# Kernel tuning notes

Hardware: AMD Instinct MI355X
Metric: run time of the kernel (lower is better)

## Reference

```python
import jax, jax.numpy as jnp
import numpy as np

EMBED_DIM = 1024
NUM_HEADS = 16
HEAD_DIM = EMBED_DIM // NUM_HEADS
MLP_HIDDEN = 4096


def layer_norm(x, gamma, beta, eps=1e-5):
    mu = jnp.mean(x, axis=-1, keepdims=True)
    var = jnp.var(x, axis=-1, keepdims=True)
    return (x - mu) / jnp.sqrt(var + eps) * gamma + beta


def setup_inputs() -> dict:
    key = jax.random.key(0)
    ks = jax.random.split(key, 16)
    d, h = EMBED_DIM, MLP_HIDDEN
    s = 0.02
    inp = {
        "x": jax.random.normal(ks[0], (2, 2048, d), dtype=jnp.float32),
        "ln1_g": jnp.ones((d,), jnp.float32),
        "ln1_b": jnp.zeros((d,), jnp.float32),
        "ln2_g": jnp.ones((d,), jnp.float32),
        "ln2_b": jnp.zeros((d,), jnp.float32),
        "Wq": jax.random.normal(ks[1], (d, d), jnp.float32) * s,
        "bq": jnp.zeros((d,), jnp.float32),
        "Wk": jax.random.normal(ks[2], (d, d), jnp.float32) * s,
        "bk": jnp.zeros((d,), jnp.float32),
        "Wv": jax.random.normal(ks[3], (d, d), jnp.float32) * s,
        "bv": jnp.zeros((d,), jnp.float32),
        "Wo": jax.random.normal(ks[4], (d, d), jnp.float32) * s,
        "bo": jnp.zeros((d,), jnp.float32),
        "W1": jax.random.normal(ks[5], (d, h), jnp.float32) * s,
        "b1": jnp.zeros((h,), jnp.float32),
        "W2": jax.random.normal(ks[6], (h, d), jnp.float32) * s,
        "b2": jnp.zeros((d,), jnp.float32),
    }
    return inp


def reference(x, ln1_g, ln1_b, ln2_g, ln2_b, Wq, bq, Wk, bk, Wv, bv, Wo, bo, W1, b1, W2, b2):
    B, T, C = x.shape
    H, Dh = NUM_HEADS, HEAD_DIM
    # attention branch
    xn = layer_norm(x, ln1_g, ln1_b)
    q = (xn @ Wq + bq).reshape(B, T, H, Dh).transpose(0, 2, 1, 3)  # [B,H,T,Dh]
    k = (xn @ Wk + bk).reshape(B, T, H, Dh).transpose(0, 2, 1, 3)
    v = (xn @ Wv + bv).reshape(B, T, H, Dh).transpose(0, 2, 1, 3)
    scores = jnp.einsum('bhtd,bhsd->bhts', q, k) / jnp.sqrt(jnp.float32(Dh))
    attn = jax.nn.softmax(scores, axis=-1)
    out = jnp.einsum('bhts,bhsd->bhtd', attn, v)
    out = out.transpose(0, 2, 1, 3).reshape(B, T, C)
    x = x + out @ Wo + bo
    # MLP branch
    xn2 = layer_norm(x, ln2_g, ln2_b)
    x = x + jax.nn.relu(xn2 @ W1 + b1) @ W2 + b2
    return x
```

## Files before the change

kernel.cpp:

```cpp
#include <hip/hip_runtime.h>

typedef float f32x4 __attribute__((ext_vector_type(4)));
typedef __bf16 bf16x8 __attribute__((ext_vector_type(8)));

constexpr int TT   = 2048;
constexpr int CC   = 1024;
constexpr int HIDN = 4096;
constexpr int MM   = 4096;
constexpr int NQKV = 3072;

union U84 { uint32_t u[4]; bf16x8 v; };

__device__ inline uint32_t cvt_pk_bf16(float lo, float hi) {
  uint32_t r;
  asm("v_cvt_pk_bf16_f32 %0, %1, %2" : "=v"(r) : "v"(lo), "v"(hi));
  return r;
}
__device__ inline ushort f2bf(float f) { return (ushort)(cvt_pk_bf16(f, 0.f) & 0xffffu); }
__device__ inline float bfbits2f(uint32_t bits) {
  union { uint32_t u; float f; } c; c.u = bits; return c.f;
}
__device__ inline float exp2_fast(float x) {
  float r;
  asm("v_exp_f32 %0, %1" : "=v"(r) : "v"(x));
  return r;
}

#define AS1C(p) ((__attribute__((address_space(1))) void*)(p))
#define AS3(p)  ((__attribute__((address_space(3))) void*)(p))

__global__ __launch_bounds__(256) void prep_weights(const float* __restrict__ Wq,
                                                    const float* __restrict__ Wk,
                                                    const float* __restrict__ Wv,
                                                    const float* __restrict__ Wo,
                                                    const float* __restrict__ W1,
                                                    const float* __restrict__ W2,
                                                    const float* __restrict__ bq,
                                                    const float* __restrict__ bk,
                                                    const float* __restrict__ bv,
                                                    const float* __restrict__ x,
                                                    const float* __restrict__ g1,
                                                    const float* __restrict__ b1v,
                                                    ushort* __restrict__ WqkvT,
                                                    ushort* __restrict__ WoT,
                                                    ushort* __restrict__ W1T,
                                                    ushort* __restrict__ W2T,
                                                    float* __restrict__ Bqkv,
                                                    ushort* __restrict__ Xn) {
  const int id = blockIdx.x;
  const int t = threadIdx.x;
  if (id >= 12300) {
    const int row = id - 12300;
    float4 v = reinterpret_cast<const float4*>(x + (size_t)row * CC)[t];
    float s  = v.x + v.y + v.z + v.w;
    float ss = v.x * v.x + v.y * v.y + v.z * v.z + v.w * v.w;
#pragma unroll
    for (int off = 32; off; off >>= 1) {
      s  += __shfl_down(s, off);
      ss += __shfl_down(ss, off);
    }
    __shared__ float red[16];
    const int wid = t >> 6, lane = t & 63;
    if (lane == 0) { red[wid] = s; red[8 + wid] = ss; }
    __syncthreads();
    if (t == 0) {
      red[0] = red[0] + red[1] + red[2] + red[3];
      red[8] = red[8] + red[9] + red[10] + red[11];
    }
    __syncthreads();
    const float mu   = red[0] * (1.0f / CC);
    const float var  = red[8] * (1.0f / CC) - mu * mu;
    const float rstd = rsqrtf(var + 1e-5f);
    float4 gg = reinterpret_cast<const float4*>(g1)[t];
    float4 bb = reinterpret_cast<const float4*>(b1v)[t];
    uint2 st;
    st.x = cvt_pk_bf16((v.x - mu) * rstd * gg.x + bb.x, (v.y - mu) * rstd * gg.y + bb.y);
    st.y = cvt_pk_bf16((v.z - mu) * rstd * gg.z + bb.z, (v.w - mu) * rstd * gg.w + bb.w);
    *reinterpret_cast<uint2*>(Xn + (size_t)row * CC + t * 4) = st;
    return;
  }
  if (id >= 12288) {
    const int i = (id - 12288) * 256 + t;
    Bqkv[i] = (i < 1024) ? bq[i] : ((i < 2048) ? bk[i - 1024] : bv[i - 2048]);
    return;
  }
  const float* W; ushort* out; int Kd, Nd, bx, by, rowOff = 0;
  if (id < 4096) {
    const int which = id >> 10, sub = id & 1023;
    bx = sub & 31; by = sub >> 5; Kd = 1024; Nd = 1024;
    if (which == 0)      { W = Wq; out = WqkvT; rowOff = 0; }
    else if (which == 1) { W = Wk; out = WqkvT; rowOff = 1024; }
    else if (which == 2) { W = Wv; out = WqkvT; rowOff = 2048; }
    else                 { W = Wo; out = WoT; }
  } else if (id < 8192) {
    const int sub = id - 4096; bx = sub & 127; by = sub >> 7;
    W = W1; out = W1T; Kd = 1024; Nd = 4096;
  } else {
    const int sub = id - 8192; bx = sub & 31; by = sub >> 5;
    W = W2; out = W2T; Kd = 4096; Nd = 1024;
  }
  const int n0 = bx * 32, k0 = by * 32;
  __shared__ float Ts[32][33];
  {
    const int r = t >> 3, cb = (t & 7) * 4;
    float4 v = *reinterpret_cast<const float4*>(W + (size_t)(k0 + r) * Nd + n0 + cb);
    Ts[r][cb + 0] = v.x; Ts[r][cb + 1] = v.y; Ts[r][cb + 2] = v.z; Ts[r][cb + 3] = v.w;
  }
  __syncthreads();
  {
    const int nl = t >> 3, kb = (t & 7) * 4;
    uint2 st;
    st.x = cvt_pk_bf16(Ts[kb + 0][nl], Ts[kb + 1][nl]);
    st.y = cvt_pk_bf16(Ts[kb + 2][nl], Ts[kb + 3][nl]);
    *reinterpret_cast<uint2*>(out + (size_t)(rowOff + n0 + nl) * Kd + k0 + kb) = st;
  }
}

template <bool RELU, bool VOUT, bool PARTIAL>
__global__ __launch_bounds__(512, 2) void gemm_8w(const ushort* __restrict__ A,
                                                  const ushort* __restrict__ Bt,
                                                  const float* __restrict__ bias,
                                                  ushort* __restrict__ outp,
                                                  ushort* __restrict__ Vt,
                                                  ushort* __restrict__ P1,
                                                  ushort* __restrict__ P2,
                                                  ushort* __restrict__ P3,
                                                  int N, int K, int Kchunk) {
  __shared__ ushort lds[49152];
  const int t = threadIdx.x, lane = t & 63, w = t >> 6;
  const int g = lane >> 4, i16 = lane & 15;
  const int wr = w >> 2, wc = w & 3;
  const int nwg  = gridDim.x * gridDim.y;
  const int orig = blockIdx.y * gridDim.x + blockIdx.x;
  const int sw   = (orig & 7) * (nwg >> 3) + (orig >> 3);
  const int row0 = (sw / gridDim.x) * 256, col0 = (sw % gridDim.x) * 256;
  const int kstart = PARTIAL ? blockIdx.z * Kchunk : 0;
  const int NT = (PARTIAL ? Kchunk : K) >> 5;
  ushort* __restrict__ Out = outp;
  if (PARTIAL) Out = (blockIdx.z == 0) ? outp : (blockIdx.z == 1) ? P1
              : (blockIdx.z == 2) ? P2 : P3;

  const int c1 = t, c2 = t + 512;
  const int r1 = c1 >> 2, s1 = (c1 & 3) ^ ((r1 >> 1) & 3);
  const int r2 = c2 >> 2, s2 = (c2 & 3) ^ ((r2 >> 1) & 3);
  const ushort* aG1 = A + (size_t)(row0 + r1) * K + kstart + s1 * 8;
  const ushort* aG2 = A + (size_t)(row0 + r2) * K + kstart + s2 * 8;
  const ushort* bG1 = Bt + (size_t)(col0 + r1) * K + kstart + s1 * 8;
  const ushort* bG2 = Bt + (size_t)(col0 + r2) * K + kstart + s2 * 8;

  int aoff[8], boff[4];
#pragma unroll
  for (int mf = 0; mf < 8; ++mf) {
    const int R = wr * 128 + mf * 16 + i16;
    aoff[mf] = R * 64 + ((g ^ ((R >> 1) & 3)) << 4);
  }
#pragma unroll
  for (int nf = 0; nf < 4; ++nf) {
    const int Cn = wc * 64 + nf * 16 + i16;
    boff[nf] = Cn * 64 + ((g ^ ((Cn >> 1) & 3)) << 4);
  }

  f32x4 acc[8][4] = {};

  auto STAGE = [&](int bi, int kt) {
    char* aB = (char*)lds + bi * 32768;
    char* bB = aB + 16384;
    const int ko = kt * 32;
    __builtin_amdgcn_global_load_lds(AS1C(aG1 + ko), AS3(aB + w * 1024), 16, 0, 0);
    __builtin_amdgcn_global_load_lds(AS1C(aG2 + ko), AS3(aB + 8192 + w * 1024), 16, 0, 0);
    __builtin_amdgcn_global_load_lds(AS1C(bG1 + ko), AS3(bB + w * 1024), 16, 0, 0);
    __builtin_amdgcn_global_load_lds(AS1C(bG2 + ko), AS3(bB + 8192 + w * 1024), 16, 0, 0);
  };

  STAGE(0, 0);
  if (NT > 1) STAGE(1, 1);

  for (int kt = 0; kt < NT; ++kt) {
    const int cur = kt % 3;
    if (kt + 2 < NT) STAGE((kt + 2) % 3, kt + 2);
    if (kt + 2 < NT)      asm volatile("s_waitcnt vmcnt(8)" ::: "memory");
    else if (kt + 1 < NT) asm volatile("s_waitcnt vmcnt(4)" ::: "memory");
    else                  asm volatile("s_waitcnt vmcnt(0)" ::: "memory");
    asm volatile("s_barrier" ::: "memory");
    __builtin_amdgcn_sched_barrier(0);

    const char* aB = (const char*)lds + cur * 32768;
    const char* bB = aB + 16384;
    bf16x8 b4[4], a4[4];
#pragma unroll
    for (int nf = 0; nf < 4; ++nf) b4[nf] = *reinterpret_cast<const bf16x8*>(bB + boff[nf]);
#pragma unroll
    for (int mf = 0; mf < 4; ++mf) a4[mf] = *reinterpret_cast<const bf16x8*>(aB + aoff[mf]);
    __builtin_amdgcn_s_setprio(1);
#pragma unroll
    for (int mf = 0; mf < 4; ++mf)
#pragma unroll
      for (int nf = 0; nf < 4; ++nf)
        acc[mf][nf] = __builtin_amdgcn_mfma_f32_16x16x32_bf16(a4[mf], b4[nf], acc[mf][nf], 0, 0, 0);
    __builtin_amdgcn_s_setprio(0);
    asm volatile("s_barrier" ::: "memory");
    __builtin_amdgcn_sched_barrier(0);
#pragma unroll
    for (int mf = 0; mf < 4; ++mf) a4[mf] = *reinterpret_cast<const bf16x8*>(aB + aoff[mf + 4]);
    __builtin_amdgcn_s_setprio(1);
#pragma unroll
    for (int mf = 0; mf < 4; ++mf)
#pragma unroll
      for (int nf = 0; nf < 4; ++nf)
        acc[mf + 4][nf] = __builtin_amdgcn_mfma_f32_16x16x32_bf16(a4[mf], b4[nf], acc[mf + 4][nf], 0, 0, 0);
    __builtin_amdgcn_s_setprio(0);
    asm volatile("s_barrier" ::: "memory");
    __builtin_amdgcn_sched_barrier(0);
  }

  const int qcol0 = col0 + wc * 64;

  if (VOUT && qcol0 >= 2048) {
#pragma unroll
    for (int nf = 0; nf < 4; ++nf) {
      const int ncol = qcol0 + nf * 16 + i16;
      const float bb = bias[ncol];
      const int d = ncol - 2048;
      const int hh = d >> 6, dd = d & 63;
#pragma unroll
      for (int mf = 0; mf < 8; ++mf) {
        const int mrow = row0 + wr * 128 + mf * 16 + 4 * g;
        const int bb_ = mrow >> 11, tok = mrow & 2047;
        uint2 st;
        st.x = cvt_pk_bf16(acc[mf][nf][0] + bb, acc[mf][nf][1] + bb);
        st.y = cvt_pk_bf16(acc[mf][nf][2] + bb, acc[mf][nf][3] + bb);
        *reinterpret_cast<uint2*>(Vt + (size_t)((bb_ * 16 + hh) * 64 + dd) * TT + tok) = st;
      }
    }
    return;
  }

  float* Lf = (float*)((char*)lds + w * 4096);
  const int rr2 = lane >> 2, q = lane & 3;
#pragma unroll
  for (int mf = 0; mf < 8; ++mf) {
#pragma unroll
    for (int nf = 0; nf < 4; ++nf)
#pragma unroll
      for (int r = 0; r < 4; ++r) {
        const int row = 4 * g + r;
        Lf[row * 64 + ((16 * nf + i16) ^ ((row & 7) << 2))] = acc[mf][nf][r];
      }
    asm volatile("s_waitcnt lgkmcnt(0)" ::: "memory");
    uint32_t u[8];
#pragma unroll
    for (int j = 0; j < 4; ++j) {
      f32x4 v = *reinterpret_cast<const f32x4*>(Lf + rr2 * 64 + ((q * 16 + 4 * j) ^ ((rr2 & 7) << 2)));
      float e0 = v[0], e1 = v[1], e2 = v[2], e3 = v[3];
      if (!PARTIAL) {
        const float4 b4 = *reinterpret_cast<const float4*>(bias + qcol0 + q * 16 + 4 * j);
        e0 += b4.x; e1 += b4.y; e2 += b4.z; e3 += b4.w;
        if (RELU) {
          e0 = fmaxf(e0, 0.f); e1 = fmaxf(e1, 0.f);
          e2 = fmaxf(e2, 0.f); e3 = fmaxf(e3, 0.f);
        }
      }
      u[2 * j + 0] = cvt_pk_bf16(e0, e1);
      u[2 * j + 1] = cvt_pk_bf16(e2, e3);
    }
    const int mrow = row0 + wr * 128 + mf * 16 + rr2;
    ushort* orow = Out + (size_t)mrow * N + qcol0 + q * 16;
    uint4 s0; s0.x = u[0]; s0.y = u[1]; s0.z = u[2]; s0.w = u[3];
    uint4 s1; s1.x = u[4]; s1.y = u[5]; s1.z = u[6]; s1.w = u[7];
    *reinterpret_cast<uint4*>(orow) = s0;
    *reinterpret_cast<uint4*>(orow + 8) = s1;
    asm volatile("s_waitcnt lgkmcnt(0)" ::: "memory");
  }
}

__global__ __launch_bounds__(256) void gemm_splitk(const ushort* __restrict__ A,
                                                   const ushort* __restrict__ Bt,
                                                   ushort* __restrict__ P0,
                                                   ushort* __restrict__ P1,
                                                   ushort* __restrict__ P2,
                                                   ushort* __restrict__ P3,
                                                   int N, int K, int Kchunk) {
  __shared__ ushort Smem[8192];
  ushort* Asm = Smem;
  ushort* Bsm = Smem + 4096;
  const int t = threadIdx.x;
  const int lane = t & 63, w = t >> 6;
  const int g = lane >> 4, i16 = lane & 15;
  const int wrow = w >> 1, wcol = w & 1;
  const int nwg  = gridDim.x * gridDim.y;
  const int orig = blockIdx.y * gridDim.x + blockIdx.x;
  const int sw   = (orig & 7) * (nwg >> 3) + (orig >> 3);
  const int row0 = (sw / gridDim.x) * 128, col0 = (sw % gridDim.x) * 128;
  const int kstart = blockIdx.z * Kchunk;
  ushort* __restrict__ P = (blockIdx.z == 0) ? P0 : (blockIdx.z == 1) ? P1
                          : (blockIdx.z == 2) ? P2 : P3;

  f32x4 acc[4][4] = {};

  const int srow = t >> 2, sc = (t & 3) * 8;
  const ushort* aS1 = A + (size_t)(row0 + srow) * K + sc;
  const ushort* aS2 = A + (size_t)(row0 + 64 + srow) * K + sc;
  const ushort* bS1 = Bt + (size_t)(col0 + srow) * K + sc;
  const ushort* bS2 = Bt + (size_t)(col0 + 64 + srow) * K + sc;
  char* aL1 = (char*)Asm + w * 1024;
  char* aL2 = (char*)Asm + 4096 + w * 1024;
  char* bL1 = (char*)Bsm + w * 1024;
  char* bL2 = (char*)Bsm + 4096 + w * 1024;

  for (int k0 = kstart; k0 < kstart + Kchunk; k0 += 32) {
    __syncthreads();
    __builtin_amdgcn_global_load_lds(AS1C(aS1 + k0), AS3(aL1), 16, 0, 0);
    __builtin_amdgcn_global_load_lds(AS1C(aS2 + k0), AS3(aL2), 16, 0, 0);
    __builtin_amdgcn_global_load_lds(AS1C(bS1 + k0), AS3(bL1), 16, 0, 0);
    __builtin_amdgcn_global_load_lds(AS1C(bS2 + k0), AS3(bL2), 16, 0, 0);
    __syncthreads();

    bf16x8 a4[4], b4[4];
#pragma unroll
    for (int mf = 0; mf < 4; ++mf) {
      const int r = wrow * 64 + mf * 16 + i16;
      a4[mf] = *reinterpret_cast<const bf16x8*>((const char*)Asm + r * 64 + g * 16);
    }
#pragma unroll
    for (int nf = 0; nf < 4; ++nf) {
      const int c = wcol * 64 + nf * 16 + i16;
      b4[nf] = *reinterpret_cast<const bf16x8*>((const char*)Bsm + c * 64 + g * 16);
    }
#pragma unroll
    for (int mf = 0; mf < 4; ++mf)
#pragma unroll
      for (int nf = 0; nf < 4; ++nf)
        acc[mf][nf] = __builtin_amdgcn_mfma_f32_16x16x32_bf16(a4[mf], b4[nf], acc[mf][nf], 0, 0, 0);
  }

  __syncthreads();

  float* Lf = (float*)((char*)Smem + w * 4096);
  const int qcol0 = col0 + wcol * 64;
  const int rr = lane >> 2, q = lane & 3;
#pragma unroll
  for (int mf = 0; mf < 4; ++mf) {
#pragma unroll
    for (int nf = 0; nf < 4; ++nf)
#pragma unroll
      for (int r = 0; r < 4; ++r) {
        const int row = 4 * g + r;
        Lf[row * 64 + ((16 * nf + i16) ^ ((row & 7) << 2))] = acc[mf][nf][r];
      }
    asm volatile("s_waitcnt lgkmcnt(0)" ::: "memory");
    uint32_t u[8];
#pragma unroll
    for (int j = 0; j < 4; ++j) {
      f32x4 v = *reinterpret_cast<const f32x4*>(Lf + rr * 64 + ((q * 16 + 4 * j) ^ ((rr & 7) << 2)));
      u[2 * j + 0] = cvt_pk_bf16(v[0], v[1]);
      u[2 * j + 1] = cvt_pk_bf16(v[2], v[3]);
    }
    const int mrow = row0 + wrow * 64 + mf * 16 + rr;
    ushort* orow = P + (size_t)mrow * N + qcol0 + q * 16;
    uint4 s0; s0.x = u[0]; s0.y = u[1]; s0.z = u[2]; s0.w = u[3];
    uint4 s1; s1.x = u[4]; s1.y = u[5]; s1.z = u[6]; s1.w = u[7];
    *reinterpret_cast<uint4*>(orow) = s0;
    *reinterpret_cast<uint4*>(orow + 8) = s1;
    asm volatile("s_waitcnt lgkmcnt(0)" ::: "memory");
  }
}

__device__ inline float bfsum4(uint32_t a, uint32_t b, uint32_t c, uint32_t d, bool hi) {
  if (hi) return bfbits2f(a & 0xffff0000u) + bfbits2f(b & 0xffff0000u) +
                 bfbits2f(c & 0xffff0000u) + bfbits2f(d & 0xffff0000u);
  return bfbits2f(a << 16) + bfbits2f(b << 16) + bfbits2f(c << 16) + bfbits2f(d << 16);
}

__global__ __launch_bounds__(256) void reduce_wo_ln(const ushort* __restrict__ P0,
                                                    const ushort* __restrict__ P1,
                                                    const ushort* __restrict__ P2,
                                                    const ushort* __restrict__ P3,
                                                    const float* __restrict__ x,
                                                    const float* __restrict__ bo,
                                                    const float* __restrict__ g,
                                                    const float* __restrict__ b,
                                                    float* __restrict__ X1f,
                                                    ushort* __restrict__ Xn) {
  const int row = blockIdx.x, t = threadIdx.x;
  const size_t off = (size_t)row * CC + t * 4;
  float4 v  = *reinterpret_cast<const float4*>(x + off);
  const uint2 q0 = *reinterpret_cast<const uint2*>(P0 + off);
  const uint2 q1 = *reinterpret_cast<const uint2*>(P1 + off);
  const uint2 q2 = *reinterpret_cast<const uint2*>(P2 + off);
  const uint2 q3 = *reinterpret_cast<const uint2*>(P3 + off);
  float4 bb = reinterpret_cast<const float4*>(bo)[t];
  v.x += bfsum4(q0.x, q1.x, q2.x, q3.x, false) + bb.x;
  v.y += bfsum4(q0.x, q1.x, q2.x, q3.x, true)  + bb.y;
  v.z += bfsum4(q0.y, q1.y, q2.y, q3.y, false) + bb.z;
  v.w += bfsum4(q0.y, q1.y, q2.y, q3.y, true)  + bb.w;
  *reinterpret_cast<float4*>(X1f + off) = v;

  float s  = v.x + v.y + v.z + v.w;
  float ss = v.x * v.x + v.y * v.y + v.z * v.z + v.w * v.w;
#pragma unroll
  for (int o = 32; o; o >>= 1) {
    s  += __shfl_down(s, o);
    ss += __shfl_down(ss, o);
  }
  __shared__ float red[16];
  const int wid = t >> 6, lane = t & 63;
  if (lane == 0) { red[wid] = s; red[8 + wid] = ss; }
  __syncthreads();
  if (t == 0) {
    red[0] = red[0] + red[1] + red[2] + red[3];
    red[8] = red[8] + red[9] + red[10] + red[11];
  }
  __syncthreads();
  const float mu   = red[0] * (1.0f / CC);
  const float var  = red[8] * (1.0f / CC) - mu * mu;
  const float rstd = rsqrtf(var + 1e-5f);
  float4 gg = reinterpret_cast<const float4*>(g)[t];
  float4 lb = reinterpret_cast<const float4*>(b)[t];
  uint2 st;
  st.x = cvt_pk_bf16((v.x - mu) * rstd * gg.x + lb.x, (v.y - mu) * rstd * gg.y + lb.y);
  st.y = cvt_pk_bf16((v.z - mu) * rstd * gg.z + lb.z, (v.w - mu) * rstd * gg.w + lb.w);
  *reinterpret_cast<uint2*>(Xn + off) = st;
}

__global__ __launch_bounds__(256) void reduce_fc2(const ushort* __restrict__ P0,
                                                  const ushort* __restrict__ P1,
                                                  const ushort* __restrict__ P2,
                                                  const ushort* __restrict__ P3,
                                                  const float* __restrict__ X1,
                                                  const float* __restrict__ b2,
                                                  float* __restrict__ out) {
  const int row = blockIdx.x, t = threadIdx.x;
  const size_t off = (size_t)row * CC + t * 4;
  float4 v  = *reinterpret_cast<const float4*>(X1 + off);
  const uint2 q0 = *reinterpret_cast<const uint2*>(P0 + off);
  const uint2 q1 = *reinterpret_cast<const uint2*>(P1 + off);
  const uint2 q2 = *reinterpret_cast<const uint2*>(P2 + off);
  const uint2 q3 = *reinterpret_cast<const uint2*>(P3 + off);
  float4 bb = reinterpret_cast<const float4*>(b2)[t];
  v.x += bfsum4(q0.x, q1.x, q2.x, q3.x, false) + bb.x;
  v.y += bfsum4(q0.x, q1.x, q2.x, q3.x, true)  + bb.y;
  v.z += bfsum4(q0.y, q1.y, q2.y, q3.y, false) + bb.z;
  v.w += bfsum4(q0.y, q1.y, q2.y, q3.y, true)  + bb.w;
  *reinterpret_cast<float4*>(out + off) = v;
}

__global__ __launch_bounds__(512, 4) void attn_partial(const ushort* __restrict__ qkv,
                                                       const ushort* __restrict__ Vt,
                                                       ushort* __restrict__ O0,
                                                       ushort* __restrict__ O1,
                                                       float2* __restrict__ ml) {
  __shared__ ushort Ks[2][4096];
  __shared__ ushort Vs[2][4096];
  __shared__ uint32_t Ps[8][16][36];
  const int t = threadIdx.x, lane = t & 63, w = t >> 6;
  const int g = lane >> 4, iq = lane & 15;
  const int flat = blockIdx.x;
  const int work = (flat & 7) * 64 + (flat >> 3);
  const int bh = work >> 4;
  const int rem = work & 15;
  const int z = rem >> 3;
  const int qt = rem & 7;
  const int b = bh >> 4, h = bh & 15;
  ushort* __restrict__ Obuf = z ? O1 : O0;

  bf16x8 qfrag[2][2];
#pragma unroll
  for (int qh = 0; qh < 2; ++qh) {
    const ushort* qrow = qkv + (size_t)(b * TT + qt * 256 + w * 32 + qh * 16 + iq) * NQKV + h * 64;
    const float qs = 0.125f * 1.44269504f;
#pragma unroll
    for (int kk = 0; kk < 2; ++kk) {
      uint4 raw = *reinterpret_cast<const uint4*>(qrow + kk * 32 + g * 8);
      uint32_t rr[4] = {raw.x, raw.y, raw.z, raw.w};
      U84 tmp;
#pragma unroll
      for (int c = 0; c < 4; ++c) {
        float lo = bfbits2f(rr[c] << 16) * qs;
        float hi = bfbits2f(rr[c] & 0xffff0000u) * qs;
        tmp.u[c] = cvt_pk_bf16(lo, hi);
      }
      qfrag[qh][kk] = tmp.v;
    }
  }

  const int sr1 = t >> 3, sc1 = t & 7;
  const int csw = (sc1 ^ (sr1 & 7)) * 8;
  const ushort* kbase = qkv + 1024 + h * 64;
  const ushort* vbase = Vt + (size_t)(bh * 64) * TT;

  auto STAGE = [&](int bi, int kt) {
    const size_t tok = (size_t)(b * TT + kt * 64);
    __builtin_amdgcn_global_load_lds(AS1C(kbase + (tok + sr1) * NQKV + csw),
                                     AS3((char*)&Ks[bi][0] + w * 1024), 16, 0, 0);
    __builtin_amdgcn_global_load_lds(AS1C(vbase + (size_t)sr1 * TT + kt * 64 + csw),
                                     AS3((char*)&Vs[bi][0] + w * 1024), 16, 0, 0);
  };

  uint32_t (*pw)[36] = Ps[w];
  const int wsw = (iq & 8) << 1;
  const int xsb = wsw << 2;
  const char* prow = (const char*)&pw[iq][0];

  float mrun[2] = {-3e38f, -3e38f}, lrun[2] = {0.f, 0.f};
  f32x4 ot[2][4] = {};

  const int kt0 = z * 16, ktE = kt0 + 16;
  STAGE(0, kt0);

  for (int kt = kt0; kt < ktE; ++kt) {
    const int cur = kt & 1;
    if (kt + 1 < ktE) {
      STAGE(cur ^ 1, kt + 1);
      asm volatile("s_waitcnt vmcnt(2)" ::: "memory");
    } else {
      asm volatile("s_waitcnt vmcnt(0)" ::: "memory");
    }
    asm volatile("s_barrier" ::: "memory");
    __builtin_amdgcn_sched_barrier(0);
    const char* Kc = (const char*)&Ks[cur][0];
    const char* Vc = (const char*)&Vs[cur][0];

#pragma unroll
    for (int qh = 0; qh < 2; ++qh) {
      f32x4 sfr[4] = {};
      __builtin_amdgcn_s_setprio(1);
#pragma unroll
      for (int kk = 0; kk < 2; ++kk)
#pragma unroll
        for (int jf = 0; jf < 4; ++jf) {
          const int row = iq + 16 * jf;
          const int off = row * 128 + ((kk * 64 + g * 16) ^ ((row & 7) << 4));
          bf16x8 a = *reinterpret_cast<const bf16x8*>(Kc + off);
          sfr[jf] = __builtin_amdgcn_mfma_f32_16x16x32_bf16(a, qfrag[qh][kk], sfr[jf], 0, 0, 0);
        }
      __builtin_amdgcn_s_setprio(0);

      float tm0 = fmaxf(fmaxf(sfr[0][0], sfr[0][1]), fmaxf(sfr[0][2], sfr[0][3]));
      float tm1 = fmaxf(fmaxf(sfr[1][0], sfr[1][1]), fmaxf(sfr[1][2], sfr[1][3]));
      float tm2 = fmaxf(fmaxf(sfr[2][0], sfr[2][1]), fmaxf(sfr[2][2], sfr[2][3]));
      float tm3 = fmaxf(fmaxf(sfr[3][0], sfr[3][1]), fmaxf(sfr[3][2], sfr[3][3]));
      float tmax = fmaxf(fmaxf(tm0, tm1), fmaxf(tm2, tm3));
      tmax = fmaxf(tmax, __shfl_xor(tmax, 16, 64));
      tmax = fmaxf(tmax, __shfl_xor(tmax, 32, 64));

      if (!__all(tmax <= mrun[qh] + 8.f)) {
        const float mnew  = fmaxf(mrun[qh], tmax);
        const float alpha = exp2_fast(mrun[qh] - mnew);
        lrun[qh] *= alpha;
#pragma unroll
        for (int df = 0; df < 4; ++df)
#pragma unroll
          for (int r = 0; r < 4; ++r) ot[qh][df][r] *= alpha;
        mrun[qh] = mnew;
      }

#pragma unroll
      for (int f = 0; f < 4; ++f) {
        float p0 = exp2_fast(sfr[f][0] - mrun[qh]);
        float p1 = exp2_fast(sfr[f][1] - mrun[qh]);
        float p2 = exp2_fast(sfr[f][2] - mrun[qh]);
        float p3 = exp2_fast(sfr[f][3] - mrun[qh]);
        lrun[qh] += (p0 + p1) + (p2 + p3);
        pw[iq][(8 * f + 2 * g + 0) ^ wsw] = cvt_pk_bf16(p0, p1);
        pw[iq][(8 * f + 2 * g + 1) ^ wsw] = cvt_pk_bf16(p2, p3);
      }
      asm volatile("s_waitcnt lgkmcnt(0)" ::: "memory");

      __builtin_amdgcn_s_setprio(1);
#pragma unroll
      for (int kk = 0; kk < 2; ++kk) {
        bf16x8 pb = *reinterpret_cast<const bf16x8*>(prow + ((kk * 64 + g * 16) ^ xsb));
#pragma unroll
        for (int df = 0; df < 4; ++df) {
          const int row = iq + 16 * df;
          const int off = row * 128 + ((kk * 64 + g * 16) ^ ((row & 7) << 4));
          bf16x8 a = *reinterpret_cast<const bf16x8*>(Vc + off);
          ot[qh][df] = __builtin_amdgcn_mfma_f32_16x16x32_bf16(a, pb, ot[qh][df], 0, 0, 0);
        }
      }
      __builtin_amdgcn_s_setprio(0);
    }

    asm volatile("s_barrier" ::: "memory");
    __builtin_amdgcn_sched_barrier(0);
  }

#pragma unroll
  for (int qh = 0; qh < 2; ++qh) {
    float l = lrun[qh];
    l += __shfl_xor(l, 16, 64);
    l += __shfl_xor(l, 32, 64);
    const int grow = b * TT + qt * 256 + w * 32 + qh * 16 + iq;
    const float inv = 1.f / l;
    ushort* orow = Obuf + (size_t)grow * CC + h * 64;
#pragma unroll
    for (int df = 0; df < 4; ++df) {
      uint2 st;
      st.x = cvt_pk_bf16(ot[qh][df][0] * inv, ot[qh][df][1] * inv);
      st.y = cvt_pk_bf16(ot[qh][df][2] * inv, ot[qh][df][3] * inv);
      *reinterpret_cast<uint2*>(orow + df * 16 + g * 4) = st;
    }
    if (g == 0) ml[(size_t)z * (MM * 16) + (size_t)grow * 16 + h] = make_float2(mrun[qh], l);
  }
}

__global__ __launch_bounds__(256) void attn_combine(const ushort* __restrict__ O0,
                                                    const ushort* __restrict__ O1,
                                                    const float2* __restrict__ ml,
                                                    ushort* __restrict__ attnb) {
  const int row = blockIdx.x, t = threadIdx.x;
  const int h = t >> 4;
  const float2 a = ml[(size_t)row * 16 + h];
  const float2 c = ml[(size_t)MM * 16 + (size_t)row * 16 + h];
  const float m  = fmaxf(a.x, c.x);
  const float w0 = exp2_fast(a.x - m) * a.y;
  const float w1 = exp2_fast(c.x - m) * c.y;
  const float inv = 1.f / (w0 + w1);
  const float s0 = w0 * inv, s1 = w1 * inv;
  const size_t off = (size_t)row * CC + t * 4;
  const uint2 r0 = *reinterpret_cast<const uint2*>(O0 + off);
  const uint2 r1 = *reinterpret_cast<const uint2*>(O1 + off);
  const float o0 = bfbits2f(r0.x << 16)         * s0 + bfbits2f(r1.x << 16)         * s1;
  const float o1 = bfbits2f(r0.x & 0xffff0000u) * s0 + bfbits2f(r1.x & 0xffff0000u) * s1;
  const float o2 = bfbits2f(r0.y << 16)         * s0 + bfbits2f(r1.y << 16)         * s1;
  const float o3 = bfbits2f(r0.y & 0xffff0000u) * s0 + bfbits2f(r1.y & 0xffff0000u) * s1;
  uint2 st;
  st.x = cvt_pk_bf16(o0, o1);
  st.y = cvt_pk_bf16(o2, o3);
  *reinterpret_cast<uint2*>(attnb + off) = st;
}

extern "C" void kernel_launch(void* const* d_in, const int* in_sizes, int n_in,
                              void* d_out, int out_size, void* d_ws, size_t ws_size,
                              hipStream_t stream) {
  const float* x     = (const float*)d_in[0];
  const float* ln1_g = (const float*)d_in[1];
  const float* ln1_b = (const float*)d_in[2];
  const float* ln2_g = (const float*)d_in[3];
  const float* ln2_b = (const float*)d_in[4];
  const float* Wq = (const float*)d_in[5];
  const float* bq = (const float*)d_in[6];
  const float* Wk = (const float*)d_in[7];
  const float* bk = (const float*)d_in[8];
  const float* Wv = (const float*)d_in[9];
  const float* bv = (const float*)d_in[10];
  const float* Wo = (const float*)d_in[11];
  const float* bo = (const float*)d_in[12];
  const float* W1 = (const float*)d_in[13];
  const float* b1 = (const float*)d_in[14];
  const float* W2 = (const float*)d_in[15];
  const float* b2 = (const float*)d_in[16];
  float* out = (float*)d_out;
  char* ws = (char*)d_ws;

  ushort* WqkvT = (ushort*)(ws + 0);
  ushort* WoT   = (ushort*)(ws + 6291456);
  ushort* W1T   = (ushort*)(ws + 8388608);
  ushort* W2T   = (ushort*)(ws + 16777216);
  float*  Bqkv  = (float*) (ws + 25165824);
  ushort* Xn    = (ushort*)(ws + 25178112);
  ushort* Attn  = (ushort*)(ws + 33566720);
  float*  X1f   = (float*) (ws + 41955328);
  ushort* Qkv   = (ushort*)(ws + 58732544);
  ushort* Vtb   = (ushort*)(ws + 83898368);
  ushort* Hid   = (ushort*)(ws + 58732544);
  ushort* OP0   = (ushort*)(ws + 41955328);
  ushort* OP1   = (ushort*)(ws + 50343936);
  float2* mlbuf = (float2*)(ws + 0);
  ushort* WoP0  = (ushort*)(ws + 58732544);
  ushort* WoP1  = (ushort*)(ws + 67121152);
  ushort* WoP2  = (ushort*)(ws + 75509760);
  ushort* WoP3  = (ushort*)(ws + 83898368);
  ushort* F2P0  = (ushort*)(ws + 0);
  ushort* F2P1  = (ushort*)(ws + 8388608);
  ushort* F2P2  = (ushort*)(ws + 25178112);
  ushort* F2P3  = (ushort*)(ws + 33566720);

  const dim3 blk(256);

  prep_weights<<<dim3(16396), blk, 0, stream>>>(Wq, Wk, Wv, Wo, W1, W2, bq, bk, bv,
                                                x, ln1_g, ln1_b,
                                                WqkvT, WoT, W1T, W2T, Bqkv, Xn);
  gemm_8w<false, true, false><<<dim3(12, 16), dim3(512), 0, stream>>>(
      Xn, WqkvT, Bqkv, Qkv, Vtb, nullptr, nullptr, nullptr, NQKV, 1024, 0);
  attn_partial<<<dim3(512), dim3(512), 0, stream>>>(Qkv, Vtb, OP0, OP1, mlbuf);
  attn_combine<<<dim3(MM), blk, 0, stream>>>(OP0, OP1, mlbuf, Attn);
  gemm_splitk<<<dim3(8, 32, 4), blk, 0, stream>>>(Attn, WoT, WoP0, WoP1, WoP2, WoP3, 1024, 1024, 256);
  reduce_wo_ln<<<dim3(MM), blk, 0, stream>>>(WoP0, WoP1, WoP2, WoP3, x, bo, ln2_g, ln2_b, X1f, Xn);
  gemm_8w<true, false, false><<<dim3(16, 16), dim3(512), 0, stream>>>(
      Xn, W1T, b1, Hid, nullptr, nullptr, nullptr, nullptr, HIDN, 1024, 0);
  gemm_8w<false, false, true><<<dim3(4, 16, 4), dim3(512), 0, stream>>>(
      Hid, W2T, nullptr, F2P0, nullptr, F2P1, F2P2, F2P3, 1024, 4096, 1024);
  reduce_fc2<<<dim3(MM), blk, 0, stream>>>(F2P0, F2P1, F2P2, F2P3, X1f, b2, out);
}
```

Before: 255.9 us.

## Load attention K/V fragments directly from global memory, dropping LDS staging

Removes the double-buffered LDS staging of K and V tiles along with its barriers. Each wave now loads its K and V MFMA fragments straight from global memory into registers, and both query halves share one set of K fragments for the score MFMAs. This cuts LDS traffic and block-wide synchronisation, but each of the 8 waves issues its own redundant global loads of the same K/V tile. It also adds register pressure and loses the prefetch overlap that the double buffer provided.

Measured after the change: 343.3 us. 34.1% more time.

```diff
diff --git a/kernel.cpp b/kernel.cpp
--- a/kernel.cpp
+++ b/kernel.cpp
@@ -449,8 +449,6 @@
                                                        ushort* __restrict__ O0,
                                                        ushort* __restrict__ O1,
                                                        float2* __restrict__ ml) {
-  __shared__ ushort Ks[2][4096];
-  __shared__ ushort Vs[2][4096];
   __shared__ uint32_t Ps[8][16][36];
   const int t = threadIdx.x, lane = t & 63, w = t >> 6;
   const int g = lane >> 4, iq = lane & 15;
@@ -483,18 +481,8 @@
     }
   }
 
-  const int sr1 = t >> 3, sc1 = t & 7;
-  const int csw = (sc1 ^ (sr1 & 7)) * 8;
-  const ushort* kbase = qkv + 1024 + h * 64;
-  const ushort* vbase = Vt + (size_t)(bh * 64) * TT;
-
-  auto STAGE = [&](int bi, int kt) {
-    const size_t tok = (size_t)(b * TT + kt * 64);
-    __builtin_amdgcn_global_load_lds(AS1C(kbase + (tok + sr1) * NQKV + csw),
-                                     AS3((char*)&Ks[bi][0] + w * 1024), 16, 0, 0);
-    __builtin_amdgcn_global_load_lds(AS1C(vbase + (size_t)sr1 * TT + kt * 64 + csw),
-                                     AS3((char*)&Vs[bi][0] + w * 1024), 16, 0, 0);
-  };
+  const ushort* kW = qkv + 1024 + h * 64 + (size_t)(b * TT + iq) * NQKV + g * 8;
+  const ushort* vW = Vt + (size_t)(bh * 64 + iq) * TT + g * 8;
 
   uint32_t (*pw)[36] = Ps[w];
   const int wsw = (iq & 8) << 1;
@@ -505,40 +493,41 @@
   f32x4 ot[2][4] = {};
 
   const int kt0 = z * 16, ktE = kt0 + 16;
-  STAGE(0, kt0);
-
   for (int kt = kt0; kt < ktE; ++kt) {
-    const int cur = kt & 1;
-    if (kt + 1 < ktE) {
-      STAGE(cur ^ 1, kt + 1);
-      asm volatile("s_waitcnt vmcnt(2)" ::: "memory");
-    } else {
-      asm volatile("s_waitcnt vmcnt(0)" ::: "memory");
-    }
-    asm volatile("s_barrier" ::: "memory");
-    __builtin_amdgcn_sched_barrier(0);
-    const char* Kc = (const char*)&Ks[cur][0];
-    const char* Vc = (const char*)&Vs[cur][0];
+    const size_t kbase = (size_t)(kt * 64) * NQKV;
+    const int vbase = kt * 64;
+
+    bf16x8 kf[8];
+#pragma unroll
+    for (int kk = 0; kk < 2; ++kk)
+#pragma unroll
+      for (int jf = 0; jf < 4; ++jf)
+        kf[kk * 4 + jf] = *reinterpret_cast<const bf16x8*>(kW + kbase + (size_t)(16 * jf) * NQKV + kk * 32);
+
+    f32x4 sfr[2][4] = {};
+    __builtin_amdgcn_s_setprio(1);
+#pragma unroll
+    for (int kk = 0; kk < 2; ++kk)
+#pragma unroll
+      for (int jf = 0; jf < 4; ++jf) {
+        sfr[0][jf] = __builtin_amdgcn_mfma_f32_16x16x32_bf16(kf[kk * 4 + jf], qfrag[0][kk], sfr[0][jf], 0, 0, 0);
+        sfr[1][jf] = __builtin_amdgcn_mfma_f32_16x16x32_bf16(kf[kk * 4 + jf], qfrag[1][kk], sfr[1][jf], 0, 0, 0);
+      }
+    __builtin_amdgcn_s_setprio(0);
+
+    bf16x8 vf[8];
+#pragma unroll
+    for (int kk = 0; kk < 2; ++kk)
+#pragma unroll
+      for (int df = 0; df < 4; ++df)
+        vf[kk * 4 + df] = *reinterpret_cast<const bf16x8*>(vW + (size_t)(16 * df) * TT + vbase + kk * 32);
 
 #pragma unroll
     for (int qh = 0; qh < 2; ++qh) {
-      f32x4 sfr[4] = {};
-      __builtin_amdgcn_s_setprio(1);
-#pragma unroll
-      for (int kk = 0; kk < 2; ++kk)
-#pragma unroll
-        for (int jf = 0; jf < 4; ++jf) {
-          const int row = iq + 16 * jf;
-          const int off = row * 128 + ((kk * 64 + g * 16) ^ ((row & 7) << 4));
-          bf16x8 a = *reinterpret_cast<const bf16x8*>(Kc + off);
-          sfr[jf] = __builtin_amdgcn_mfma_f32_16x16x32_bf16(a, qfrag[qh][kk], sfr[jf], 0, 0, 0);
-        }
-      __builtin_amdgcn_s_setprio(0);
-
-      float tm0 = fmaxf(fmaxf(sfr[0][0], sfr[0][1]), fmaxf(sfr[0][2], sfr[0][3]));
-      float tm1 = fmaxf(fmaxf(sfr[1][0], sfr[1][1]), fmaxf(sfr[1][2], sfr[1][3]));
-      float tm2 = fmaxf(fmaxf(sfr[2][0], sfr[2][1]), fmaxf(sfr[2][2], sfr[2][3]));
-      float tm3 = fmaxf(fmaxf(sfr[3][0], sfr[3][1]), fmaxf(sfr[3][2], sfr[3][3]));
+      float tm0 = fmaxf(fmaxf(sfr[qh][0][0], sfr[qh][0][1]), fmaxf(sfr[qh][0][2], sfr[qh][0][3]));
+      float tm1 = fmaxf(fmaxf(sfr[qh][1][0], sfr[qh][1][1]), fmaxf(sfr[qh][1][2], sfr[qh][1][3]));
+      float tm2 = fmaxf(fmaxf(sfr[qh][2][0], sfr[qh][2][1]), fmaxf(sfr[qh][2][2], sfr[qh][2][3]));
+      float tm3 = fmaxf(fmaxf(sfr[qh][3][0], sfr[qh][3][1]), fmaxf(sfr[qh][3][2], sfr[qh][3][3]));
       float tmax = fmaxf(fmaxf(tm0, tm1), fmaxf(tm2, tm3));
       tmax = fmaxf(tmax, __shfl_xor(tmax, 16, 64));
       tmax = fmaxf(tmax, __shfl_xor(tmax, 32, 64));
@@ -556,10 +545,10 @@
 
 #pragma unroll
       for (int f = 0; f < 4; ++f) {
-        float p0 = exp2_fast(sfr[f][0] - mrun[qh]);
-        float p1 = exp2_fast(sfr[f][1] - mrun[qh]);
-        float p2 = exp2_fast(sfr[f][2] - mrun[qh]);
-        float p3 = exp2_fast(sfr[f][3] - mrun[qh]);
+        float p0 = exp2_fast(sfr[qh][f][0] - mrun[qh]);
+        float p1 = exp2_fast(sfr[qh][f][1] - mrun[qh]);
+        float p2 = exp2_fast(sfr[qh][f][2] - mrun[qh]);
+        float p3 = exp2_fast(sfr[qh][f][3] - mrun[qh]);
         lrun[qh] += (p0 + p1) + (p2 + p3);
         pw[iq][(8 * f + 2 * g + 0) ^ wsw] = cvt_pk_bf16(p0, p1);
         pw[iq][(8 * f + 2 * g + 1) ^ wsw] = cvt_pk_bf16(p2, p3);
@@ -571,18 +560,11 @@
       for (int kk = 0; kk < 2; ++kk) {
         bf16x8 pb = *reinterpret_cast<const bf16x8*>(prow + ((kk * 64 + g * 16) ^ xsb));
 #pragma unroll
-        for (int df = 0; df < 4; ++df) {
-          const int row = iq + 16 * df;
-          const int off = row * 128 + ((kk * 64 + g * 16) ^ ((row & 7) << 4));
-          bf16x8 a = *reinterpret_cast<const bf16x8*>(Vc + off);
-          ot[qh][df] = __builtin_amdgcn_mfma_f32_16x16x32_bf16(a, pb, ot[qh][df], 0, 0, 0);
-        }
+        for (int df = 0; df < 4; ++df)
+          ot[qh][df] = __builtin_amdgcn_mfma_f32_16x16x32_bf16(vf[kk * 4 + df], pb, ot[qh][df], 0, 0, 0);
       }
       __builtin_amdgcn_s_setprio(0);
     }
-
-    asm volatile("s_barrier" ::: "memory");
-    __builtin_amdgcn_sched_barrier(0);
   }
 
 #pragma unroll
```
